# Performance work log

Measured on AMD Instinct MI355X. Metric: run time of the kernel, lower is better.

## Reference

```python
import jax, jax.numpy as jnp
import numpy as np


def setup_inputs() -> dict:
    key = jax.random.key(0)
    ks = jax.random.split(key, 6)
    B, S, D, F, E = 4, 2048, 512, 2048, 8
    scale = 0.02
    return {
        "x": jax.random.normal(ks[0], (B, S, D), dtype=jnp.float32),
        "gate_w": jax.random.normal(ks[1], (D, E), dtype=jnp.float32) * scale,
        "w1": jax.random.normal(ks[2], (E, D, F), dtype=jnp.float32) * scale,
        "b1": jax.random.normal(ks[3], (E, F), dtype=jnp.float32) * scale,
        "w2": jax.random.normal(ks[4], (E, F, D), dtype=jnp.float32) * scale,
        "b2": jax.random.normal(ks[5], (E, D), dtype=jnp.float32) * scale,
    }


TOP_K = 2


def reference(x, gate_w, w1, b1, w2, b2):
    E = w1.shape[0]
    orig_shape = x.shape
    xr = x.reshape(-1, x.shape[-1])              # [T, D]

    # Router
    logits = xr @ gate_w                          # [T, E]
    probs = jax.nn.softmax(logits, axis=-1)
    mean_probs = probs.mean(axis=0)               # [E]
    load_balance_loss = E * jnp.sum(mean_probs * mean_probs)

    topw, topi = jax.lax.top_k(probs, TOP_K)      # [T, K]
    topw = topw / jnp.sum(topw, axis=-1, keepdims=True)

    # Per-token combine weight per expert: sum over top-k slots of weight * one-hot
    combine = jnp.sum(jax.nn.one_hot(topi, E, dtype=xr.dtype) * topw[..., None], axis=1)  # [T, E]

    # Dense per-expert FFN (equivalent math to the permute/slice dispatch:
    # each selected token gets expert_e(x) scaled by its normalized router weight).
    hidden = jax.nn.gelu(jnp.einsum("td,edf->etf", xr, w1) + b1[:, None, :], approximate=False)  # [E, T, F]
    outs = jnp.einsum("etf,efd->etd", hidden, w2) + b2[:, None, :]                               # [E, T, D]

    y = jnp.einsum("etd,te->td", outs, combine)   # [T, D]
    return y.reshape(orig_shape), load_balance_loss
```

## Files before the change

kernel.cpp:

```cpp
#include <hip/hip_runtime.h>
#include <stdint.h>

#define T_TOKENS 8192
#define D_DIM 512
#define F_DIM 2048
#define E_NUM 8

typedef short short8 __attribute__((ext_vector_type(8)));
typedef short s16x4 __attribute__((ext_vector_type(4)));
typedef float f32x4 __attribute__((ext_vector_type(4)));

__device__ __forceinline__ unsigned short f2bf(float f) {
    union { float f; unsigned int u; } c; c.f = f;
    unsigned int u = c.u;
    unsigned int r = (u + 0x7fffu + ((u >> 16) & 1u)) >> 16;
    return (unsigned short)r;
}
__device__ __forceinline__ unsigned int pack2(float a, float b) {
    return (unsigned int)f2bf(a) | ((unsigned int)f2bf(b) << 16);
}
__device__ __forceinline__ float gelu_fast(float h) {
    float a = h * fmaf(h * h, -0.1029433f, -2.3022141f);
    return h * __builtin_amdgcn_rcpf(1.f + __builtin_amdgcn_exp2f(a));
}

#define SLOT_CAP 17408
#define WS_COUNT 0
#define WS_PROBS 512
#define WS_TOK   16384
#define WS_WGT   (WS_TOK + E_NUM * T_TOKENS * 4)
#define WS_INV   (WS_WGT + E_NUM * T_TOKENS * 4)
#define WS_W1B   (1ull << 20)
#define WS_W2B   (WS_W1B + 16777216ull)
#define WS_XG    (WS_W2B + 16777216ull)
#define WS_HG    (WS_XG + (unsigned long long)SLOT_CAP * D_DIM * 2)
#define WS_OG    (WS_HG + (unsigned long long)SLOT_CAP * F_DIM * 2)
#define OG_BYTES ((unsigned long long)SLOT_CAP * D_DIM * 4)

__device__ __forceinline__ void expert_off(const int* __restrict__ count, int e,
                                           int& off_e, int& cnt_e) {
    int off = 0, ce = 0;
#pragma unroll
    for (int i = 0; i < E_NUM; ++i) {
        int c = count[i];
        if (i == e) ce = c;
        if (i < e) off += (c + 127) & ~127;
    }
    off_e = off; cnt_e = ce;
}

__global__ __launch_bounds__(256) void moe_convert(
    const float* __restrict__ w1, const float* __restrict__ w2,
    unsigned short* __restrict__ w1b, unsigned short* __restrict__ w2b,
    int* __restrict__ count, float* __restrict__ probs_g)
{
    __shared__ float ts[32][65];
    int tid = threadIdx.x;
    if (blockIdx.x == 0 && tid < E_NUM) { count[tid] = 0; probs_g[tid] = 0.f; }

    int b = blockIdx.x;
    bool is2 = b >= 4096;
    int o = is2 ? b - 4096 : b;
    int e = o >> 9, r = o & 511;
    int N  = is2 ? 512 : 2048;
    int Ks = is2 ? 64 : 16;
    int ng, ks;
    if (!is2) { ng = r & 31; ks = r >> 5; }
    else      { ng = r & 7;  ks = r >> 3; }

    const float* src = (is2 ? w2 : w1) + ((size_t)e << 20) + (size_t)(ks * 32) * N + ng * 64;
    int row = tid >> 3, c4 = (tid & 7) * 4;
    f32x4 v0 = *(const f32x4*)(src + (size_t)row * N + c4);
    f32x4 v1 = *(const f32x4*)(src + (size_t)row * N + c4 + 32);
    *(f32x4*)&ts[row][c4] = v0;
    *(f32x4*)&ts[row][c4 + 32] = v1;
    __syncthreads();

    int f = tid >> 6, L = tid & 63, q = L >> 4, n = L & 15;
    float v[8];
#pragma unroll
    for (int j = 0; j < 8; ++j) v[j] = ts[q * 8 + j][f * 16 + n];
    uint4 pk;
    pk.x = pack2(v[0], v[1]); pk.y = pack2(v[2], v[3]);
    pk.z = pack2(v[4], v[5]); pk.w = pack2(v[6], v[7]);
    size_t fraglane = ((size_t)((e * (N / 16) + ng * 4 + f) * Ks + ks)) * 64 + L;
    unsigned short* dst = (is2 ? w2b : w1b) + fraglane * 8;
    *(uint4*)dst = pk;
}

__global__ __launch_bounds__(256) void moe_router(
    const float* __restrict__ x, const float* __restrict__ gw,
    int* __restrict__ count, int* __restrict__ tok_list,
    float* __restrict__ wgt_list, float* __restrict__ probs_g,
    int* __restrict__ inv)
{
    __shared__ float pprob[E_NUM];
    __shared__ int   lcnt[E_NUM];
    __shared__ int   gbase[E_NUM];
    __shared__ int   ltok[E_NUM][64];
    __shared__ float lwgt[E_NUM][64];
    __shared__ unsigned char re1[32], re2[32];
    __shared__ short rs1[32], rs2[32];

    int tid = threadIdx.x;
    if (tid < E_NUM) { pprob[tid] = 0.f; lcnt[tid] = 0; }
    __syncthreads();

    int wv = tid >> 6, lane = tid & 63;

    float gr[64];
    {
        const f32x4* gp = (const f32x4*)(gw + lane * 64);
#pragma unroll
        for (int i = 0; i < 16; ++i) *(f32x4*)&gr[i * 4] = gp[i];
    }

    float wps[E_NUM];
#pragma unroll
    for (int e = 0; e < E_NUM; ++e) wps[e] = 0.f;

#pragma unroll 1
    for (int i = 0; i < 8; ++i) {
        int t = blockIdx.x * 32 + wv * 8 + i;
        const float* xp = x + (size_t)t * D_DIM + lane * 8;
        f32x4 x0 = *(const f32x4*)xp;
        f32x4 x1 = *(const f32x4*)(xp + 4);
        float xv[8] = { x0.x, x0.y, x0.z, x0.w, x1.x, x1.y, x1.z, x1.w };
        float acc[E_NUM];
#pragma unroll
        for (int e = 0; e < E_NUM; ++e) acc[e] = 0.f;
#pragma unroll
        for (int j = 0; j < 8; ++j)
#pragma unroll
            for (int e = 0; e < E_NUM; ++e) acc[e] += xv[j] * gr[j * 8 + e];
#pragma unroll
        for (int off = 1; off < 64; off <<= 1)
#pragma unroll
            for (int e = 0; e < E_NUM; ++e) acc[e] += __shfl_xor(acc[e], off);

        float m = acc[0];
#pragma unroll
        for (int e = 1; e < E_NUM; ++e) m = fmaxf(m, acc[e]);
        float p[E_NUM], s = 0.f;
#pragma unroll
        for (int e = 0; e < E_NUM; ++e) { p[e] = __expf(acc[e] - m); s += p[e]; }
        float invs = 1.f / s;
#pragma unroll
        for (int e = 0; e < E_NUM; ++e) { p[e] *= invs; wps[e] += p[e]; }

        int e1 = 0;
#pragma unroll
        for (int e = 1; e < E_NUM; ++e) if (p[e] > p[e1]) e1 = e;
        int e2 = (e1 == 0) ? 1 : 0;
#pragma unroll
        for (int e = 0; e < E_NUM; ++e) if (e != e1 && p[e] > p[e2]) e2 = e;

        if (lane == 0) {
            float invw = 1.f / (p[e1] + p[e2]);
            int s1 = atomicAdd(&lcnt[e1], 1); ltok[e1][s1] = t; lwgt[e1][s1] = p[e1] * invw;
            int s2 = atomicAdd(&lcnt[e2], 1); ltok[e2][s2] = t; lwgt[e2][s2] = p[e2] * invw;
            int li = wv * 8 + i;
            re1[li] = (unsigned char)e1; rs1[li] = (short)s1;
            re2[li] = (unsigned char)e2; rs2[li] = (short)s2;
        }
    }
    if (lane == 0) {
#pragma unroll
        for (int e = 0; e < E_NUM; ++e) atomicAdd(&pprob[e], wps[e]);
    }
    __syncthreads();
    if (tid < E_NUM) {
        gbase[tid] = atomicAdd(&count[tid], lcnt[tid]);
        atomicAdd(&probs_g[tid], pprob[tid]);
    }
    __syncthreads();
    if (tid < 32) {
        int t = blockIdx.x * 32 + tid;
        inv[t * 2]     = ((int)re1[tid] << 16) | (gbase[re1[tid]] + rs1[tid]);
        inv[t * 2 + 1] = ((int)re2[tid] << 16) | (gbase[re2[tid]] + rs2[tid]);
    }
    int ee = tid >> 5;
    for (int ss = tid & 31; ss < lcnt[ee]; ss += 32) {
        int dst = ee * T_TOKENS + gbase[ee] + ss;
        tok_list[dst] = ltok[ee][ss];
        wgt_list[dst] = lwgt[ee][ss];
    }
}

__global__ __launch_bounds__(256) void moe_gather(
    const float* __restrict__ x, const int* __restrict__ count,
    const int* __restrict__ tok_list, unsigned short* __restrict__ Xg,
    const float* __restrict__ probs_g, float* __restrict__ y)
{
    if (blockIdx.x == 0 && threadIdx.x == 0) {
        float s = 0.f;
#pragma unroll
        for (int i = 0; i < E_NUM; ++i) {
            float m = probs_g[i] / (float)T_TOKENS;
            s += m * m;
        }
        y[(size_t)T_TOKENS * D_DIM] = (float)E_NUM * s;
    }

    int e = blockIdx.x & 7, tile = blockIdx.x >> 3;
    int off_e, cnt;
    expert_off(count, e, off_e, cnt);
    int padcnt = (cnt + 127) & ~127;
    if (tile * 64 >= padcnt) return;

    int tid = threadIdx.x;
    int tl = tid >> 2;
    int kq = tid & 3;
    int slot = tile * 64 + tl;
    bool valid = slot < cnt;
    int tok = valid ? tok_list[e * T_TOKENS + slot] : 0;
    const float* xr = x + (size_t)tok * D_DIM + kq * 128;
    int base16 = ((off_e + tile * 64) >> 4) + (tl >> 4);
    int mlane = tl & 15;

#pragma unroll 4
    for (int g = 0; g < 16; ++g) {
        uint4 pk;
        if (valid) {
            f32x4 v0 = *(const f32x4*)(xr + g * 8);
            f32x4 v1 = *(const f32x4*)(xr + g * 8 + 4);
            pk.x = pack2(v0.x, v0.y); pk.y = pack2(v0.z, v0.w);
            pk.z = pack2(v1.x, v1.y); pk.w = pack2(v1.z, v1.w);
        } else {
            pk.x = 0; pk.y = 0; pk.z = 0; pk.w = 0;
        }
        int kb = kq * 4 + (g >> 2);
        int lane = mlane + 16 * (g & 3);
        *(uint4*)(Xg + ((size_t)(base16 * 16 + kb) * 64 + lane) * 8) = pk;
    }
}

__global__ __launch_bounds__(256) void moe_gemm1(
    const unsigned short* __restrict__ Xg, const unsigned short* __restrict__ w1b,
    const float* __restrict__ b1, const int* __restrict__ count,
    unsigned short* __restrict__ Hg)
{
    int l = (blockIdx.x & 7) * 1024 + (blockIdx.x >> 3);
    int e = l >> 10;
    int rem = l & 1023;
    int mt = rem >> 4, nt = rem & 15;
    int off_e, cnt;
    expert_off(count, e, off_e, cnt);
    if (mt * 128 >= cnt) return;

    int tid = threadIdx.x;
    int wv = tid >> 6, lane = tid & 63;
    int wh = wv >> 1, nh = wv & 1;
    int q = lane >> 4, n = lane & 15;

    int slot16b = (off_e >> 4) + mt * 8 + wh * 4;
    const short8* Ap = (const short8*)Xg + (size_t)slot16b * 1024 + lane;
    const short8* Bp = (const short8*)w1b + (size_t)(e * 128 + nt * 8 + nh * 4) * 1024 + lane;

    f32x4 acc[4][4];
#pragma unroll
    for (int j = 0; j < 4; ++j)
#pragma unroll
        for (int i = 0; i < 4; ++i) acc[j][i] = (f32x4){0.f, 0.f, 0.f, 0.f};

#pragma unroll 2
    for (int ks = 0; ks < 16; ++ks) {
        short8 A[4], B[4];
#pragma unroll
        for (int i = 0; i < 4; ++i) A[i] = Ap[(size_t)i * 1024 + ks * 64];
#pragma unroll
        for (int j = 0; j < 4; ++j) B[j] = Bp[(size_t)j * 1024 + ks * 64];
#pragma unroll
        for (int j = 0; j < 4; ++j)
#pragma unroll
            for (int i = 0; i < 4; ++i)
                acc[j][i] = __builtin_amdgcn_mfma_f32_16x16x32_bf16(B[j], A[i], acc[j][i], 0, 0, 0);
    }

    s16x4* Hg8 = (s16x4*)Hg;
    int q1 = q >> 1, q0 = q & 1;
#pragma unroll
    for (int j = 0; j < 4; ++j) {
        f32x4 bb = *(const f32x4*)(b1 + e * F_DIM + nt * 128 + nh * 64 + j * 16 + q * 4);
        int ftile = nt * 8 + nh * 4 + j;
#pragma unroll
        for (int i = 0; i < 4; ++i) {
            s16x4 sv;
#pragma unroll
            for (int rr = 0; rr < 4; ++rr)
                sv[rr] = (short)f2bf(gelu_fast(acc[j][i][rr] + bb[rr]));
            Hg8[(size_t)(slot16b + i) * 8192 + ftile * 64 + q1 * 32 + 2 * n + q0] = sv;
        }
    }
}

__global__ __launch_bounds__(256) void moe_gemm2(
    const unsigned short* __restrict__ Hg, const unsigned short* __restrict__ w2b,
    const float* __restrict__ b2, const int* __restrict__ count,
    const float* __restrict__ wgt_list, float* __restrict__ Og0,
    float* __restrict__ Og1, int ksplit)
{
    int e, kt, mt, nt;
    if (ksplit) {
        int l = (blockIdx.x & 7) * 1024 + (blockIdx.x >> 3);
        e = l >> 10;
        int rem = l & 1023;
        mt = rem >> 3; kt = (rem >> 2) & 1; nt = rem & 3;
    } else {
        int l = (blockIdx.x & 7) * 512 + (blockIdx.x >> 3);
        e = l >> 9;
        int rem = l & 511;
        mt = rem >> 2; kt = 0; nt = rem & 3;
    }
    int off_e, cnt;
    expert_off(count, e, off_e, cnt);
    if (mt * 64 >= cnt) return;

    __shared__ float swgt[64];

    int tid = threadIdx.x;
    if (tid < 64) {
        int s = mt * 64 + tid;
        swgt[tid] = (s < cnt) ? wgt_list[e * T_TOKENS + s] : 0.f;
    }
    __syncthreads();

    int wv = tid >> 6, lane = tid & 63;
    int wh = wv >> 1, nh = wv & 1;
    int q = lane >> 4, n = lane & 15;

    int nkb = ksplit ? 32 : 64;
    int kb0 = kt * 32;

    int slot16b = (off_e >> 4) + mt * 4 + wh * 2;
    const short8* Ap = (const short8*)Hg + (size_t)slot16b * 4096 + kb0 * 64 + lane;
    const short8* Bp = (const short8*)w2b + (size_t)(e * 32 + nt * 8 + nh * 4) * 4096 + kb0 * 64 + lane;

    f32x4 acc[4][2];
#pragma unroll
    for (int j = 0; j < 4; ++j)
#pragma unroll
        for (int i = 0; i < 2; ++i) acc[j][i] = (f32x4){0.f, 0.f, 0.f, 0.f};

    short8 Acur0 = Ap[0], Acur1 = Ap[4096];

#pragma unroll 2
    for (int kb = 0; kb < nkb; ++kb) {
        short8 Anxt0, Anxt1;
        if (kb + 1 < nkb) {
            Anxt0 = Ap[(kb + 1) * 64];
            Anxt1 = Ap[4096 + (kb + 1) * 64];
        }
        short8 B[4];
#pragma unroll
        for (int j = 0; j < 4; ++j) B[j] = Bp[(size_t)j * 4096 + kb * 64];
#pragma unroll
        for (int j = 0; j < 4; ++j) {
            acc[j][0] = __builtin_amdgcn_mfma_f32_16x16x32_bf16(B[j], Acur0, acc[j][0], 0, 0, 0);
            acc[j][1] = __builtin_amdgcn_mfma_f32_16x16x32_bf16(B[j], Acur1, acc[j][1], 0, 0, 0);
        }
        if (kb + 1 < nkb) { Acur0 = Anxt0; Acur1 = Anxt1; }
    }

    float* Og = (kt == 0) ? Og0 : Og1;
#pragma unroll
    for (int j = 0; j < 4; ++j) {
        int d0 = nt * 128 + nh * 64 + j * 16 + q * 4;
        f32x4 bb;
        if (kt == 0) bb = *(const f32x4*)(b2 + e * D_DIM + d0);
        else         bb = (f32x4){0.f, 0.f, 0.f, 0.f};
#pragma unroll
        for (int i = 0; i < 2; ++i) {
            int m = wh * 32 + i * 16 + n;
            float wg = swgt[m];
            f32x4 o;
#pragma unroll
            for (int rr = 0; rr < 4; ++rr) o[rr] = wg * (acc[j][i][rr] + bb[rr]);
            *(f32x4*)(Og + (size_t)(off_e + mt * 64 + m) * D_DIM + d0) = o;
        }
    }
}

__global__ __launch_bounds__(256) void moe_combine(
    const float* __restrict__ Og0, const float* __restrict__ Og1,
    const int* __restrict__ inv, const int* __restrict__ count,
    float* __restrict__ y, int ksplit)
{
    __shared__ int offs[E_NUM];
    int tid = threadIdx.x;
    if (tid < E_NUM) {
        int off = 0;
        for (int i = 0; i < tid; ++i) off += (count[i] + 127) & ~127;
        offs[tid] = off;
    }
    __syncthreads();

    int tk = blockIdx.x * 2 + (tid >> 7);
    int l = tid & 127;
    int i1 = inv[tk * 2], i2 = inv[tk * 2 + 1];
    size_t r1 = (size_t)(offs[i1 >> 16] + (i1 & 0xffff)) * D_DIM;
    size_t r2 = (size_t)(offs[i2 >> 16] + (i2 & 0xffff)) * D_DIM;
    f32x4 a = *((const f32x4*)(Og0 + r1) + l);
    f32x4 b = *((const f32x4*)(Og0 + r2) + l);
    f32x4 o = { a.x + b.x, a.y + b.y, a.z + b.z, a.w + b.w };
    if (ksplit) {
        f32x4 c = *((const f32x4*)(Og1 + r1) + l);
        f32x4 d = *((const f32x4*)(Og1 + r2) + l);
        o.x += c.x + d.x; o.y += c.y + d.y; o.z += c.z + d.z; o.w += c.w + d.w;
    }
    *((f32x4*)(y + (size_t)tk * D_DIM) + l) = o;
}

extern "C" void kernel_launch(void* const* d_in, const int* in_sizes, int n_in,
                              void* d_out, int out_size, void* d_ws, size_t ws_size,
                              hipStream_t stream) {
    const float* x  = (const float*)d_in[0];
    const float* gw = (const float*)d_in[1];
    const float* w1 = (const float*)d_in[2];
    const float* b1 = (const float*)d_in[3];
    const float* w2 = (const float*)d_in[4];
    const float* b2 = (const float*)d_in[5];
    float* out = (float*)d_out;

    char* ws = (char*)d_ws;
    int*   count     = (int*)(ws + WS_COUNT);
    float* probs_g   = (float*)(ws + WS_PROBS);
    int*   tok_list  = (int*)(ws + WS_TOK);
    float* wgt_list  = (float*)(ws + WS_WGT);
    int*   inv       = (int*)(ws + WS_INV);
    unsigned short* w1b = (unsigned short*)(ws + WS_W1B);
    unsigned short* w2b = (unsigned short*)(ws + WS_W2B);
    unsigned short* Xg  = (unsigned short*)(ws + WS_XG);
    unsigned short* Hg  = (unsigned short*)(ws + WS_HG);
    float*          Og0 = (float*)(ws + WS_OG);
    float*          Og1 = (float*)(ws + WS_OG + OG_BYTES);

    int ksplit = (ws_size >= WS_OG + 2 * OG_BYTES) ? 1 : 0;

    moe_convert<<<8192, 256, 0, stream>>>(w1, w2, w1b, w2b, count, probs_g);
    moe_router<<<T_TOKENS / 32, 256, 0, stream>>>(x, gw, count, tok_list, wgt_list, probs_g, inv);
    moe_gather<<<8 * 128, 256, 0, stream>>>(x, count, tok_list, Xg, probs_g, out);
    moe_gemm1<<<8 * 64 * 16, 256, 0, stream>>>(Xg, w1b, b1, count, Hg);
    moe_gemm2<<<(ksplit ? 8192 : 4096), 256, 0, stream>>>(Hg, w2b, b2, count, wgt_list, Og0, Og1, ksplit);
    moe_combine<<<T_TOKENS / 2, 256, 0, stream>>>(Og0, Og1, inv, count, out, ksplit);
}
```

Baseline: 300.0 us.

## Stage GEMM tiles through LDS via direct global-to-LDS loads; enlarge gemm2 M tile

Both expert GEMMs now copy the A and B tiles into shared memory with global_load_lds, and the four waves of a block share them, instead of each wave loading its own fragments straight from global memory. Each tile is fetched once per block rather than once per wave, which cuts global and L2 traffic. gemm2's M tile grows from 64 to 128 rows with a 4x4 accumulator per wave, halving the grid. In exchange the code adds two barriers per k-step with no double buffering, so loads do not overlap compute, and uses 32KB of LDS per block, which may lower occupancy.

```diff
diff --git a/kernel.cpp b/kernel.cpp
--- a/kernel.cpp
+++ b/kernel.cpp
@@ -22,6 +22,11 @@
 __device__ __forceinline__ float gelu_fast(float h) {
     float a = h * fmaf(h * h, -0.1029433f, -2.3022141f);
     return h * __builtin_amdgcn_rcpf(1.f + __builtin_amdgcn_exp2f(a));
+}
+__device__ __forceinline__ void gload_lds16(const void* g, void* l) {
+    __builtin_amdgcn_global_load_lds(
+        (const __attribute__((address_space(1))) void*)g,
+        (__attribute__((address_space(3))) void*)l, 16, 0, 0);
 }
 
 #define SLOT_CAP 17408
@@ -248,14 +253,17 @@
     expert_off(count, e, off_e, cnt);
     if (mt * 128 >= cnt) return;
 
+    __shared__ __align__(16) unsigned short Alds[8192];
+    __shared__ __align__(16) unsigned short Blds[8192];
+
     int tid = threadIdx.x;
     int wv = tid >> 6, lane = tid & 63;
     int wh = wv >> 1, nh = wv & 1;
     int q = lane >> 4, n = lane & 15;
 
-    int slot16b = (off_e >> 4) + mt * 8 + wh * 4;
-    const short8* Ap = (const short8*)Xg + (size_t)slot16b * 1024 + lane;
-    const short8* Bp = (const short8*)w1b + (size_t)(e * 128 + nt * 8 + nh * 4) * 1024 + lane;
+    int slot16b = (off_e >> 4) + mt * 8;
+    const short8* Ag = (const short8*)Xg + (size_t)slot16b * 1024;
+    const short8* Bg = (const short8*)w1b + (size_t)(e * 128 + nt * 8) * 1024;
 
     f32x4 acc[4][4];
 #pragma unroll
@@ -263,22 +271,40 @@
 #pragma unroll
         for (int i = 0; i < 4; ++i) acc[j][i] = (f32x4){0.f, 0.f, 0.f, 0.f};
 
-#pragma unroll 2
-    for (int ks = 0; ks < 16; ++ks) {
-        short8 A[4], B[4];
-#pragma unroll
-        for (int i = 0; i < 4; ++i) A[i] = Ap[(size_t)i * 1024 + ks * 64];
-#pragma unroll
-        for (int j = 0; j < 4; ++j) B[j] = Bp[(size_t)j * 1024 + ks * 64];
-#pragma unroll
-        for (int j = 0; j < 4; ++j)
+#pragma unroll 1
+    for (int kt = 0; kt < 8; ++kt) {
+#pragma unroll
+        for (int rr = 0; rr < 8; ++rr) {
+            int idx = wv * 8 + rr;
+            int isB = idx >> 4;
+            int s = (idx & 15) >> 1, kbi = idx & 1;
+            const short8* g = (isB ? Bg : Ag) + (size_t)s * 1024 + (kt * 2 + kbi) * 64 + lane;
+            unsigned short* ld = (isB ? Blds : Alds) + (size_t)((s * 2 + kbi) * 64) * 8;
+            gload_lds16((const void*)g, (void*)ld);
+        }
+        __syncthreads();
+
+#pragma unroll
+        for (int kbi = 0; kbi < 2; ++kbi) {
+            short8 A[4], B[4];
 #pragma unroll
             for (int i = 0; i < 4; ++i)
-                acc[j][i] = __builtin_amdgcn_mfma_f32_16x16x32_bf16(B[j], A[i], acc[j][i], 0, 0, 0);
+                A[i] = *(const short8*)(Alds + (size_t)((((wh * 4 + i) * 2 + kbi) * 64 + lane)) * 8);
+#pragma unroll
+            for (int j = 0; j < 4; ++j)
+                B[j] = *(const short8*)(Blds + (size_t)((((nh * 4 + j) * 2 + kbi) * 64 + lane)) * 8);
+#pragma unroll
+            for (int j = 0; j < 4; ++j)
+#pragma unroll
+                for (int i = 0; i < 4; ++i)
+                    acc[j][i] = __builtin_amdgcn_mfma_f32_16x16x32_bf16(B[j], A[i], acc[j][i], 0, 0, 0);
+        }
+        __syncthreads();
     }
 
     s16x4* Hg8 = (s16x4*)Hg;
     int q1 = q >> 1, q0 = q & 1;
+    int slot16w = slot16b + wh * 4;
 #pragma unroll
     for (int j = 0; j < 4; ++j) {
         f32x4 bb = *(const f32x4*)(b1 + e * F_DIM + nt * 128 + nh * 64 + j * 16 + q * 4);
@@ -289,7 +315,7 @@
 #pragma unroll
             for (int rr = 0; rr < 4; ++rr)
                 sv[rr] = (short)f2bf(gelu_fast(acc[j][i][rr] + bb[rr]));
-            Hg8[(size_t)(slot16b + i) * 8192 + ftile * 64 + q1 * 32 + 2 * n + q0] = sv;
+            Hg8[(size_t)(slot16w + i) * 8192 + ftile * 64 + q1 * 32 + 2 * n + q0] = sv;
         }
     }
 }
@@ -302,64 +328,77 @@
 {
     int e, kt, mt, nt;
     if (ksplit) {
-        int l = (blockIdx.x & 7) * 1024 + (blockIdx.x >> 3);
-        e = l >> 10;
-        int rem = l & 1023;
-        mt = rem >> 3; kt = (rem >> 2) & 1; nt = rem & 3;
-    } else {
         int l = (blockIdx.x & 7) * 512 + (blockIdx.x >> 3);
         e = l >> 9;
         int rem = l & 511;
+        mt = rem >> 3; kt = (rem >> 2) & 1; nt = rem & 3;
+    } else {
+        int l = (blockIdx.x & 7) * 256 + (blockIdx.x >> 3);
+        e = l >> 8;
+        int rem = l & 255;
         mt = rem >> 2; kt = 0; nt = rem & 3;
     }
     int off_e, cnt;
     expert_off(count, e, off_e, cnt);
-    if (mt * 64 >= cnt) return;
-
-    __shared__ float swgt[64];
-
-    int tid = threadIdx.x;
-    if (tid < 64) {
-        int s = mt * 64 + tid;
+    if (mt * 128 >= cnt) return;
+
+    __shared__ __align__(16) unsigned short Alds[8192];
+    __shared__ __align__(16) unsigned short Blds[8192];
+    __shared__ float swgt[128];
+
+    int tid = threadIdx.x;
+    if (tid < 128) {
+        int s = mt * 128 + tid;
         swgt[tid] = (s < cnt) ? wgt_list[e * T_TOKENS + s] : 0.f;
     }
-    __syncthreads();
 
     int wv = tid >> 6, lane = tid & 63;
     int wh = wv >> 1, nh = wv & 1;
     int q = lane >> 4, n = lane & 15;
 
-    int nkb = ksplit ? 32 : 64;
+    int nsteps = ksplit ? 16 : 32;
     int kb0 = kt * 32;
 
-    int slot16b = (off_e >> 4) + mt * 4 + wh * 2;
-    const short8* Ap = (const short8*)Hg + (size_t)slot16b * 4096 + kb0 * 64 + lane;
-    const short8* Bp = (const short8*)w2b + (size_t)(e * 32 + nt * 8 + nh * 4) * 4096 + kb0 * 64 + lane;
-
-    f32x4 acc[4][2];
+    int slot16b = (off_e >> 4) + mt * 8;
+    const short8* Ag = (const short8*)Hg + (size_t)slot16b * 4096;
+    const short8* Bg = (const short8*)w2b + (size_t)(e * 32 + nt * 8) * 4096;
+
+    f32x4 acc[4][4];
 #pragma unroll
     for (int j = 0; j < 4; ++j)
 #pragma unroll
-        for (int i = 0; i < 2; ++i) acc[j][i] = (f32x4){0.f, 0.f, 0.f, 0.f};
-
-    short8 Acur0 = Ap[0], Acur1 = Ap[4096];
-
-#pragma unroll 2
-    for (int kb = 0; kb < nkb; ++kb) {
-        short8 Anxt0, Anxt1;
-        if (kb + 1 < nkb) {
-            Anxt0 = Ap[(kb + 1) * 64];
-            Anxt1 = Ap[4096 + (kb + 1) * 64];
-        }
-        short8 B[4];
-#pragma unroll
-        for (int j = 0; j < 4; ++j) B[j] = Bp[(size_t)j * 4096 + kb * 64];
-#pragma unroll
-        for (int j = 0; j < 4; ++j) {
-            acc[j][0] = __builtin_amdgcn_mfma_f32_16x16x32_bf16(B[j], Acur0, acc[j][0], 0, 0, 0);
-            acc[j][1] = __builtin_amdgcn_mfma_f32_16x16x32_bf16(B[j], Acur1, acc[j][1], 0, 0, 0);
-        }
-        if (kb + 1 < nkb) { Acur0 = Anxt0; Acur1 = Anxt1; }
+        for (int i = 0; i < 4; ++i) acc[j][i] = (f32x4){0.f, 0.f, 0.f, 0.f};
+
+#pragma unroll 1
+    for (int kss = 0; kss < nsteps; ++kss) {
+#pragma unroll
+        for (int rr = 0; rr < 8; ++rr) {
+            int idx = wv * 8 + rr;
+            int isB = idx >> 4;
+            int s = (idx & 15) >> 1, kbi = idx & 1;
+            int kb = kb0 + kss * 2 + kbi;
+            const short8* g = (isB ? Bg : Ag) + (size_t)s * 4096 + kb * 64 + lane;
+            unsigned short* ld = (isB ? Blds : Alds) + (size_t)((s * 2 + kbi) * 64) * 8;
+            gload_lds16((const void*)g, (void*)ld);
+        }
+        __syncthreads();
+
+#pragma unroll
+        for (int kbi = 0; kbi < 2; ++kbi) {
+            short8 A[4], B[4];
+#pragma unroll
+            for (int i = 0; i < 4; ++i)
+                A[i] = *(const short8*)(Alds + (size_t)((((wh * 4 + i) * 2 + kbi) * 64 + lane)) * 8);
+#pragma unroll
+            for (int j = 0; j < 4; ++j)
+                B[j] = *(const short8*)(Blds + (size_t)((((nh * 4 + j) * 2 + kbi) * 64 + lane)) * 8);
+#pragma unroll
+            for (int j = 0; j < 4; ++j)
+#pragma unroll
+                for (int i = 0; i < 4; ++i)
+                    acc[j][i] = __builtin_amdgcn_mfma_f32_16x16x32_bf16(B[j], A[i], acc[j][i], 0, 0, 0);
+        }
+        __syncthreads();
     }
 
     float* Og = (kt == 0) ? Og0 : Og1;
@@ -370,13 +409,13 @@
         if (kt == 0) bb = *(const f32x4*)(b2 + e * D_DIM + d0);
         else         bb = (f32x4){0.f, 0.f, 0.f, 0.f};
 #pragma unroll
-        for (int i = 0; i < 2; ++i) {
-            int m = wh * 32 + i * 16 + n;
+        for (int i = 0; i < 4; ++i) {
+            int m = wh * 64 + i * 16 + n;
             float wg = swgt[m];
             f32x4 o;
 #pragma unroll
             for (int rr = 0; rr < 4; ++rr) o[rr] = wg * (acc[j][i][rr] + bb[rr]);
-            *(f32x4*)(Og + (size_t)(off_e + mt * 64 + m) * D_DIM + d0) = o;
+            *(f32x4*)(Og + (size_t)(off_e + mt * 128 + m) * D_DIM + d0) = o;
         }
     }
 }
@@ -440,7 +479,7 @@
     moe_convert<<<8192, 256, 0, stream>>>(w1, w2, w1b, w2b, count, probs_g);
     moe_router<<<T_TOKENS / 32, 256, 0, stream>>>(x, gw, count, tok_list, wgt_list, probs_g, inv);
     moe_gather<<<8 * 128, 256, 0, stream>>>(x, count, tok_list, Xg, probs_g, out);
-    moe_gemm1<<<8 * 64 * 16, 256, 0, stream>>>(Xg, w1b, b1, count, Hg);
-    moe_gemm2<<<(ksplit ? 8192 : 4096), 256, 0, stream>>>(Hg, w2b, b2, count, wgt_list, Og0, Og1, ksplit);
+    moe_gemm1<<<8192, 256, 0, stream>>>(Xg, w1b, b1, count, Hg);
+    moe_gemm2<<<(ksplit ? 4096 : 2048), 256, 0, stream>>>(Hg, w2b, b2, count, wgt_list, Og0, Og1, ksplit);
     moe_combine<<<T_TOKENS / 2, 256, 0, stream>>>(Og0, Og1, inv, count, out, ksplit);
 }
```

Measured after the change: 271.8 us. 9.4% less time.
